# Kernel tuning notes

Hardware: AMD Instinct MI355X
Metric: run time of the kernel (lower is better)

## Reference

```python
import jax, jax.numpy as jnp
import numpy as np
from itertools import combinations, product

NQ = 10
DIM = 2 ** NQ
DEPTH = 1
ENC_PAIRS = [(q, q + 1) for q in range(0, NQ - 1, 2)] + [(q, q + 1) for q in range(1, NQ - 1, 2)]  # brick layer: even then odd
PYR = [(i, i + 1) for layer in range(NQ - 1) for i in range(NQ - layer - 1)]  # pyramid RBS wire pairs (45)
OBS_PAIRS = list(combinations(range(NQ), 2))  # 45 pairwise 2-local observables

_P = {'I': np.eye(2, dtype=np.complex128),
      'X': np.array([[0, 1], [1, 0]], dtype=np.complex128),
      'Y': np.array([[0, -1j], [1j, 0]], dtype=np.complex128),
      'Z': np.array([[1, 0], [0, -1]], dtype=np.complex128)}
_WORDS = [''.join(w) for w in product('IXYZ', repeat=2)][1:]  # PennyLane pauli_basis order, identity excluded
P15 = jnp.asarray(np.stack([np.kron(_P[w[0]], _P[w[1]]) for w in _WORDS]).astype(np.complex64))
XXm = jnp.asarray(np.kron(_P['X'], _P['X']).astype(np.complex64))
YYm = jnp.asarray(np.kron(_P['Y'], _P['Y']).astype(np.complex64))
ZZm = jnp.asarray(np.kron(_P['Z'], _P['Z']).astype(np.complex64))
I4 = jnp.eye(4, dtype=jnp.complex64)
_TRIL_I, _TRIL_J = np.tril_indices(4, -1)  # order matches create_Hermitian's count+j indexing


def _u3(t, p, l):
    c = jnp.cos(t / 2).astype(jnp.complex64)
    s = jnp.sin(t / 2).astype(jnp.complex64)
    return jnp.stack([jnp.stack([c, -jnp.exp(1j * l) * s]),
                      jnp.stack([jnp.exp(1j * p) * s, jnp.exp(1j * (p + l)) * c])])


def _ising(phi, P):
    # exp(-i*phi/2 * P) for P in {XX, YY, ZZ} (P^2 = I)
    return jnp.cos(phi / 2) * I4 - 1j * jnp.sin(phi / 2) * P


def _apply1(psi, U, w):
    # psi: (B, 2, ..., 2); single-qubit gate U (2,2) on wire w
    psi = jnp.moveaxis(psi, 1 + w, -1)
    sh = psi.shape
    out = jnp.einsum('ij,brj->bri', U, psi.reshape(sh[0], -1, 2)).reshape(sh)
    return jnp.moveaxis(out, -1, 1 + w)


def _apply2(psi, U, a, b):
    # two-qubit gate on wires (a,b), a is most-significant (PennyLane wire order). U: (4,4) or batched (B,4,4)
    psi = jnp.moveaxis(psi, (1 + a, 1 + b), (-2, -1))
    sh = psi.shape
    flat = psi.reshape(sh[0], -1, 4)
    eq = 'bij,brj->bri' if U.ndim == 3 else 'ij,brj->bri'
    out = jnp.einsum(eq, U, flat).reshape(sh)
    return jnp.moveaxis(out, (-2, -1), (1 + a, 1 + b))


def _build_H(A, B, D):
    # create_Hermitian: lower triangle A+iB, diag[0:3] = D[1:4], diag[3]=0, then h + h^dagger
    n = A.shape[0]
    h = jnp.zeros((n, 4, 4), jnp.complex64)
    h = h.at[:, _TRIL_I, _TRIL_J].set(A.astype(jnp.complex64) + 1j * B.astype(jnp.complex64))
    d = np.arange(3)
    h = h.at[:, d, d].set(D[:, 1:4].astype(jnp.complex64))
    return h + jnp.conj(jnp.swapaxes(h, -1, -2))


def setup_inputs() -> dict:
    key = jax.random.key(0)
    ks = jax.random.split(key, 9)
    f32 = jnp.float32
    return {
        'x': jax.random.normal(ks[0], (256, 512), f32),
        'W1': jax.random.normal(ks[1], (512, 256), f32) * (512 ** -0.5),
        'b1': jnp.zeros((256,), f32),
        'W2': jax.random.normal(ks[2], (256, 135), f32) * (256 ** -0.5),
        'b2': jnp.zeros((135,), f32),
        'qvit_params': 0.01 * jax.random.normal(ks[3], (DEPTH, len(PYR), 12), f32),
        'A': 2.0 * jax.random.normal(ks[4], (len(OBS_PAIRS), 6), f32),
        'B': 2.0 * jax.random.normal(ks[5], (len(OBS_PAIRS), 6), f32),
        'D': 2.0 * jax.random.normal(ks[6], (len(OBS_PAIRS), 4), f32),
    }


def reference(x, W1, b1, W2, b2, qvit_params, A, B, D):
    Bsz = x.shape[0]
    # enc_proj: Linear -> SiLU -> Linear
    enc = jax.nn.silu(x @ W1 + b1) @ W2 + b2  # (B, 135)
    # Brick-layer SpecialUnitary encoding: U = exp(i * sum theta_m P_m) via eigh
    theta = enc.reshape(Bsz, len(ENC_PAIRS), 15).astype(jnp.complex64)
    Hg = jnp.einsum('bgm,mij->bgij', theta, P15)  # Hermitian generators (B, 9, 4, 4)
    ew, V = jnp.linalg.eigh(Hg)
    Ue = jnp.einsum('bgik,bgk,bgjk->bgij', V, jnp.exp(1j * ew.astype(jnp.complex64)), jnp.conj(V))
    # |0...0>
    psi = jnp.zeros((Bsz, DIM), jnp.complex64).at[:, 0].set(1.0).reshape((Bsz,) + (2,) * NQ)
    for g, (a, b) in enumerate(ENC_PAIRS):
        psi = _apply2(psi, Ue[:, g], a, b)
    # QViT pyramid ansatz
    for ly in range(DEPTH):
        for g, (a, b) in enumerate(PYR):
            p = qvit_params[ly, g]
            psi = _apply1(psi, _u3(p[0], p[1], p[2]), a)
            psi = _apply2(psi, _ising(p[3], XXm), a, b)
            psi = _apply2(psi, _ising(p[4], YYm), a, b)
            psi = _apply2(psi, _ising(p[5], ZZm), a, b)
            psi = _apply1(psi, _u3(p[6], p[7], p[8]), a)
            psi = _apply2(psi, _ising(p[9], XXm), a, b)
            psi = _apply2(psi, _ising(p[10], YYm), a, b)
            psi = _apply2(psi, _ising(p[11], ZZm), a, b)
    # Pairwise ANO Hermitian expectations
    Hobs = _build_H(A, B, D)  # (45, 4, 4)
    outs = []
    for w, (a, b) in enumerate(OBS_PAIRS):
        pm = jnp.moveaxis(psi, (1 + a, 1 + b), (1, 2)).reshape(Bsz, 4, -1)
        outs.append(jnp.real(jnp.einsum('bir,ij,bjr->b', jnp.conj(pm), Hobs[w], pm)))
    return jnp.stack(outs, axis=1).astype(jnp.float32)
```

## Files before the change

### kernel.cpp

```cpp
#include <hip/hip_runtime.h>
#include <math.h>

#define NOBS 45
typedef float2 c32;

__device__ __constant__ int PA_s[NOBS] = {
    1,1,1,1,1,1,1,1,1, 0,0,0,0,0,0,0,0, 7,7,7,7,7,7,7, 6,6,6,6,6,6,
    5,5,5,5,5, 3,3,3,3, 2,2,2, 4,4, 9};
__device__ __constant__ int PB_s[NOBS] = {
    0,7,6,5,3,2,4,9,8, 7,6,5,3,2,4,9,8, 6,5,3,2,4,9,8, 5,3,2,4,9,8,
    3,2,4,9,8, 2,4,9,8, 4,9,8, 9,8, 8};
constexpr int TIc[6] = {1, 2, 2, 3, 3, 3};
constexpr int TJc[6] = {0, 0, 1, 0, 1, 2};

__device__ __forceinline__ c32 cfma(c32 a, c32 b, c32 c) {
    c.x = fmaf(a.x, b.x, fmaf(-a.y, b.y, c.x));
    c.y = fmaf(a.x, b.y, fmaf(a.y, b.x, c.y));
    return c;
}
__device__ __forceinline__ c32 cmul(c32 a, c32 b) {
    return make_float2(a.x * b.x - a.y * b.y, a.x * b.y + a.y * b.x);
}

template <int CTRL>
__device__ __forceinline__ float dppf(float x) {
    return __uint_as_float((unsigned)__builtin_amdgcn_update_dpp(
        0, (int)__float_as_uint(x), CTRL, 0xF, 0xF, true));
}
__device__ __forceinline__ float swap32f(float a) {
    auto r = __builtin_amdgcn_permlane32_swap(__float_as_uint(a), __float_as_uint(a), false, false);
    return (__uint_as_float(r[0]) + __uint_as_float(r[1])) - a;
}
#if __has_builtin(__builtin_amdgcn_permlane16_swap)
__device__ __forceinline__ float swap16f(float a) {
    auto r = __builtin_amdgcn_permlane16_swap(__float_as_uint(a), __float_as_uint(a), false, false);
    return (__uint_as_float(r[0]) + __uint_as_float(r[1])) - a;
}
#else
__device__ __forceinline__ float swap16f(float a) { return __shfl_xor(a, 16, 64); }
#endif
__device__ __forceinline__ float swz4f(float a) {
    return __uint_as_float(__builtin_amdgcn_ds_swizzle(__float_as_uint(a), 0x101F));
}
template <int M>
__device__ __forceinline__ float exf(float x) {
    float r = x;
    if constexpr ((M & 3) == 1) r = dppf<0xB1>(r);
    else if constexpr ((M & 3) == 2) r = dppf<0x4E>(r);
    else if constexpr ((M & 3) == 3) r = dppf<0x1B>(r);
    if constexpr (M & 4)  r = swz4f(r);
    if constexpr (M & 8)  r = dppf<0x128>(r);
    if constexpr (M & 16) r = swap16f(r);
    if constexpr (M & 32) r = swap32f(r);
    return r;
}
template <int M>
__device__ __forceinline__ c32 exch(c32 a) { return make_float2(exf<M>(a.x), exf<M>(a.y)); }
__device__ __forceinline__ c32 swap32c(c32 a) { return make_float2(swap32f(a.x), swap32f(a.y)); }

__device__ __forceinline__ float wave_reduce63(float x) {
    x += dppf<0x111>(x);
    x += dppf<0x112>(x);
    x += dppf<0x114>(x);
    x += dppf<0x118>(x);
    x += dppf<0x142>(x);
    x += dppf<0x143>(x);
    return x;
}

__device__ __forceinline__ int insert2(int t, int pl, int ph) {
    int low  = t & ((1 << pl) - 1);
    int rest = t >> pl;
    int nm   = ph - 1 - pl;
    int mid  = rest & ((1 << nm) - 1);
    int high = rest >> nm;
    return low | (mid << (pl + 1)) | (high << (ph + 1));
}

template <int W>
__device__ __forceinline__ c32 pE(int r, int c) {
    if constexpr (W == 0) return make_float2((r == c) ? 1.f : 0.f, 0.f);
    else if constexpr (W == 1) return make_float2((r != c) ? 1.f : 0.f, 0.f);
    else if constexpr (W == 2) return make_float2(0.f, (r == c) ? 0.f : ((r == 0) ? -1.f : 1.f));
    else return make_float2((r == c) ? ((r == 0) ? 1.f : -1.f) : 0.f, 0.f);
}
template <int W0, int W1>
__device__ __forceinline__ void paccum(c32& H, float th, int i1, int i2, int j1, int j2) {
    c32 a = pE<W0>(i1, j1), b = pE<W1>(i2, j2);
    c32 p = cmul(a, b);
    H.x = fmaf(th, p.x, H.x);
    H.y = fmaf(th, p.y, H.y);
}

struct F16 { c32 u[16]; };
struct FLoc { c32 a[4]; c32 b[4]; };
struct F4 { c32 uS, uB, uA, uC; };

__device__ __forceinline__ F16 loadF16(const c32* __restrict__ U) {
    F16 f;
#pragma unroll
    for (int i = 0; i < 16; i++) f.u[i] = U[i];
    return f;
}
__device__ __forceinline__ FLoc loadLoc(const c32* __restrict__ U, int ln) {
    int bb = (ln >> 5) & 1;
    const c32* U0 = U + bb * 4;
    const c32* U1 = U + (2 | bb) * 4;
    int c00 = bb, c01 = 2 | bb, c10 = bb ^ 1, c11 = 2 | (bb ^ 1);
    FLoc f;
    f.a[0] = U0[c00]; f.a[1] = U0[c01]; f.a[2] = U0[c10]; f.a[3] = U0[c11];
    f.b[0] = U1[c00]; f.b[1] = U1[c01]; f.b[2] = U1[c10]; f.b[3] = U1[c11];
    return f;
}
template <int QA, int QB>
__device__ __forceinline__ F4 loadL2(const c32* __restrict__ U, int ln) {
    int bA = (ln >> QA) & 1, bB = (ln >> QB) & 1;
    int r = (bA << 1) | bB;
    const c32* Ur = U + r * 4;
    F4 f;
    f.uS = Ur[r]; f.uB = Ur[r ^ 1]; f.uA = Ur[r ^ 2]; f.uC = Ur[r ^ 3];
    return f;
}

__device__ __forceinline__ void applyLL(c32 v[4], const F16& f) {
    c32 n0 = cfma(f.u[0],  v[0], cfma(f.u[1],  v[1], cfma(f.u[2],  v[2], cmul(f.u[3],  v[3]))));
    c32 n1 = cfma(f.u[4],  v[0], cfma(f.u[5],  v[1], cfma(f.u[6],  v[2], cmul(f.u[7],  v[3]))));
    c32 n2 = cfma(f.u[8],  v[0], cfma(f.u[9],  v[1], cfma(f.u[10], v[2], cmul(f.u[11], v[3]))));
    c32 n3 = cfma(f.u[12], v[0], cfma(f.u[13], v[1], cfma(f.u[14], v[2], cmul(f.u[15], v[3]))));
    v[0] = n0; v[1] = n1; v[2] = n2; v[3] = n3;
}
__device__ __forceinline__ void applyLoc(c32 v[4], const FLoc& f) {
    c32 p0 = swap32c(v[0]), p1 = swap32c(v[1]), p2 = swap32c(v[2]), p3 = swap32c(v[3]);
    c32 n0 = cfma(f.a[0], v[0], cfma(f.a[1], v[1], cfma(f.a[2], p0, cmul(f.a[3], p1))));
    c32 n1 = cfma(f.b[0], v[0], cfma(f.b[1], v[1], cfma(f.b[2], p0, cmul(f.b[3], p1))));
    c32 n2 = cfma(f.a[0], v[2], cfma(f.a[1], v[3], cfma(f.a[2], p2, cmul(f.a[3], p3))));
    c32 n3 = cfma(f.b[0], v[2], cfma(f.b[1], v[3], cfma(f.b[2], p2, cmul(f.b[3], p3))));
    v[0] = n0; v[1] = n1; v[2] = n2; v[3] = n3;
}
template <int QA, int QB>
__device__ __forceinline__ void applyL2(c32 v[4], const F4& f) {
#pragma unroll
    for (int lc = 0; lc < 4; lc++) {
        c32 pB = exch<(1 << QB)>(v[lc]);
        c32 pA = exch<(1 << QA)>(v[lc]);
        c32 pC = exch<(1 << QA)>(pB);
        v[lc] = cfma(f.uS, v[lc], cfma(f.uB, pB, cfma(f.uA, pA, cmul(f.uC, pC))));
    }
}

__device__ __forceinline__ void dumpV(const c32 v[4], c32* __restrict__ psi, int t) {
#pragma unroll
    for (int lc = 0; lc < 4; lc++) psi[(t << 2) | lc] = v[lc];
}
__device__ __forceinline__ void loadV(c32 v[4], const c32* __restrict__ psi, int t) {
#pragma unroll
    for (int lc = 0; lc < 4; lc++) v[lc] = psi[(t << 2) | lc];
}
template <int PA, int PB>
__device__ __forceinline__ void ldsApply(const F16& f, c32* __restrict__ psi, int t) {
    constexpr int PL = (PA < PB) ? PA : PB, PH = (PA < PB) ? PB : PA;
    int base = insert2(t, PL, PH);
    constexpr int oa = 1 << PA, ob = 1 << PB;
    c32 g0 = psi[base], g1 = psi[base + ob], g2 = psi[base + oa], g3 = psi[base + oa + ob];
    c32 n0 = cfma(f.u[0],  g0, cfma(f.u[1],  g1, cfma(f.u[2],  g2, cmul(f.u[3],  g3))));
    c32 n1 = cfma(f.u[4],  g0, cfma(f.u[5],  g1, cfma(f.u[6],  g2, cmul(f.u[7],  g3))));
    c32 n2 = cfma(f.u[8],  g0, cfma(f.u[9],  g1, cfma(f.u[10], g2, cmul(f.u[11], g3))));
    c32 n3 = cfma(f.u[12], g0, cfma(f.u[13], g1, cfma(f.u[14], g2, cmul(f.u[15], g3))));
    psi[base] = n0; psi[base + ob] = n1; psi[base + oa] = n2; psi[base + oa + ob] = n3;
}

__global__ __launch_bounds__(256, 1) void mega_kernel(
    const float* __restrict__ x,  const float* __restrict__ W1, const float* __restrict__ b1,
    const float* __restrict__ W2, const float* __restrict__ b2, const float* __restrict__ qp,
    const float* __restrict__ Am, const float* __restrict__ Bm, const float* __restrict__ Dm,
    float* __restrict__ out) {
    __shared__ __align__(16) c32 psiS[1024];
    __shared__ c32 UeS[144];
    __shared__ c32 GpS[720];
    __shared__ float HbS[720];
    __shared__ float encS[136];
    __shared__ float redS[180];

    const int b = blockIdx.x, t = threadIdx.x, ln = t & 63;
    float* F = (float*)psiS;

    if (t < 128) ((float4*)F)[t] = ((const float4*)(x + (size_t)b * 512))[t];
    __syncthreads();
    {
        int q = t & 63, sl = t >> 6;
        float4 a4 = make_float4(0.f, 0.f, 0.f, 0.f);
#pragma unroll 16
        for (int kk = 0; kk < 128; kk++) {
            int k = sl * 128 + kk;
            float xk = F[k];
            const float4 w = *(const float4*)(W1 + (size_t)k * 256 + q * 4);
            a4.x = fmaf(xk, w.x, a4.x); a4.y = fmaf(xk, w.y, a4.y);
            a4.z = fmaf(xk, w.z, a4.z); a4.w = fmaf(xk, w.w, a4.w);
        }
        *(float4*)(F + 512 + sl * 256 + q * 4) = a4;
    }
    __syncthreads();
    {
        float hv = b1[t] + F[512 + t] + F[768 + t] + F[1024 + t] + F[1280 + t];
        hv = hv / (1.f + __expf(-hv));
        F[1536 + t] = hv;
    }
    __syncthreads();
    if (t < 135) {
        float a2 = b2[t], a3 = 0.f;
#pragma unroll 16
        for (int k = 0; k < 128; k++) {
            a2 = fmaf(F[1536 + k],       W2[(size_t)k * 135 + t],         a2);
            a3 = fmaf(F[1536 + 128 + k], W2[(size_t)(128 + k) * 135 + t], a3);
        }
        encS[t] = a2 + a3;
    }
    __syncthreads();

    c32* Mm = psiS;
    c32* Rb = psiS + 144;
    c32* TA = psiS + 288;
    if (t < 144) {
        int m = t >> 4, e = t & 15, i = e >> 2, j = e & 3;
        int i1 = i >> 1, i2 = i & 1, j1 = j >> 1, j2 = j & 1;
        const float* th = encS + m * 15;
        c32 H = make_float2(0.f, 0.f);
        paccum<0,1>(H, th[0],  i1,i2,j1,j2); paccum<0,2>(H, th[1],  i1,i2,j1,j2);
        paccum<0,3>(H, th[2],  i1,i2,j1,j2); paccum<1,0>(H, th[3],  i1,i2,j1,j2);
        paccum<1,1>(H, th[4],  i1,i2,j1,j2); paccum<1,2>(H, th[5],  i1,i2,j1,j2);
        paccum<1,3>(H, th[6],  i1,i2,j1,j2); paccum<2,0>(H, th[7],  i1,i2,j1,j2);
        paccum<2,1>(H, th[8],  i1,i2,j1,j2); paccum<2,2>(H, th[9],  i1,i2,j1,j2);
        paccum<2,3>(H, th[10], i1,i2,j1,j2); paccum<3,0>(H, th[11], i1,i2,j1,j2);
        paccum<3,1>(H, th[12], i1,i2,j1,j2); paccum<3,2>(H, th[13], i1,i2,j1,j2);
        paccum<3,3>(H, th[14], i1,i2,j1,j2);
        const float sc = 1.f / 64.f;
        Mm[t] = make_float2(-H.y * sc, H.x * sc);
        Rb[t] = make_float2((i == j) ? 1.f : 0.f, 0.f);
    } else if (t >= 234) {
        for (int w = t - 234; w < NOBS; w += 22) {
            float* Hf = HbS + w * 16;
            Hf[0] = 2.f * Dm[w * 4 + 1];
            Hf[1] = 2.f * Dm[w * 4 + 2];
            Hf[2] = 2.f * Dm[w * 4 + 3];
            Hf[3] = 0.f;
#pragma unroll
            for (int k = 0; k < 6; k++) {
                Hf[4 + 2 * k] = 2.f * Am[w * 6 + k];
                Hf[5 + 2 * k] = 2.f * Bm[w * 6 + k];
            }
        }
    }
    __syncthreads();
    c32 Mrow[4];
    if (t < 144) {
        int m = t >> 4, i = (t & 15) >> 2;
#pragma unroll
        for (int k = 0; k < 4; k++) Mrow[k] = Mm[m * 16 + i * 4 + k];
    }
#pragma unroll 1
    for (int step = 0; step < 13; step++) {
        if (t < 144) {
            int m = t >> 4, e = t & 15, i = e >> 2, j = e & 3;
            const c32* cur = (step & 1) ? UeS : Rb;
            c32 acc = make_float2(0.f, 0.f);
            c32 outv;
            if (step < 7) {
#pragma unroll
                for (int k = 0; k < 4; k++) acc = cfma(Mrow[k], cur[m * 16 + k * 4 + j], acc);
                float inv = 1.f / (float)(7 - step);
                outv = make_float2(fmaf(acc.x, inv, (i == j) ? 1.f : 0.f), acc.y * inv);
            } else {
#pragma unroll
                for (int k = 0; k < 4; k++)
                    acc = cfma(cur[m * 16 + i * 4 + k], cur[m * 16 + k * 4 + j], acc);
                outv = acc;
            }
            ((step & 1) ? Rb : UeS)[t] = outv;
        } else if (t >= 144 && t < 234 && step < 8) {
            int pt = t - 144, g = pt >> 1, ih = (pt & 1) << 1;
            const float* p = qp + g * 12;
            const c32* src = ((step & 1) ? TA : GpS) + g * 16;
            c32* dst = ((step & 1) ? GpS : TA) + g * 16;
#pragma unroll
            for (int r2 = 0; r2 < 2; r2++) {
                int i = ih + r2, i1 = i >> 1, i2 = i & 1;
                c32 row[4];
                if (step == 0) {
                    float s, c; __sincosf(p[0] * 0.5f, &s, &c);
                    c32 u0, u1;
                    if (i1 == 0) { u0 = make_float2(c, 0.f);
                                   u1 = make_float2(-__cosf(p[2]) * s, -__sinf(p[2]) * s); }
                    else { u0 = make_float2(__cosf(p[1]) * s, __sinf(p[1]) * s);
                           u1 = make_float2(__cosf(p[1] + p[2]) * c, __sinf(p[1] + p[2]) * c); }
#pragma unroll
                    for (int jj = 0; jj < 4; jj++) row[jj] = make_float2(0.f, 0.f);
                    row[i2] = u0; row[2 | i2] = u1;
                } else {
                    c32 coef0, coef1; int c0, c1;
                    if (step == 1 || step == 5) {
                        float s, c; __sincosf(p[step == 1 ? 3 : 9] * 0.5f, &s, &c);
                        c0 = i; coef0 = make_float2(c, 0.f);
                        c1 = i ^ 3; coef1 = make_float2(0.f, -s);
                    } else if (step == 2 || step == 6) {
                        float s, c; __sincosf(p[step == 2 ? 4 : 10] * 0.5f, &s, &c);
                        float yy = (i == 0 || i == 3) ? 1.f : -1.f;
                        c0 = i; coef0 = make_float2(c, 0.f);
                        c1 = i ^ 3; coef1 = make_float2(0.f, s * yy);
                    } else if (step == 3 || step == 7) {
                        float s, c; __sincosf(p[step == 3 ? 5 : 11] * 0.5f, &s, &c);
                        float zz = (i == 0 || i == 3) ? 1.f : -1.f;
                        c0 = i; coef0 = make_float2(c, -s * zz);
                        c1 = i; coef1 = make_float2(0.f, 0.f);
                    } else {
                        float s, c; __sincosf(p[6] * 0.5f, &s, &c);
                        if (i1 == 0) { coef0 = make_float2(c, 0.f);
                                       coef1 = make_float2(-__cosf(p[8]) * s, -__sinf(p[8]) * s); }
                        else { coef0 = make_float2(__cosf(p[7]) * s, __sinf(p[7]) * s);
                               coef1 = make_float2(__cosf(p[7] + p[8]) * c, __sinf(p[7] + p[8]) * c); }
                        c0 = i2; c1 = 2 | i2;
                    }
#pragma unroll
                    for (int jj = 0; jj < 4; jj++)
                        row[jj] = cfma(coef0, src[c0 * 4 + jj], cmul(coef1, src[c1 * 4 + jj]));
                }
#pragma unroll
                for (int jj = 0; jj < 4; jj++) dst[i * 4 + jj] = row[jj];
            }
        }
        __syncthreads();
    }

    c32 v[4];
#pragma unroll
    for (int lc = 0; lc < 4; lc++) v[lc] = make_float2(0.f, 0.f);
    if (t == 0) v[0] = make_float2(1.f, 0.f);

    applyLL(v, loadF16(UeS + 0));
    applyL2<5, 4>(v, loadL2<5, 4>(UeS + 16, ln));
    applyL2<3, 1>(v, loadL2<3, 1>(UeS + 32, ln));
    applyL2<0, 2>(v, loadL2<0, 2>(UeS + 48, ln));
    dumpV(v, psiS, t); __syncthreads();
    ldsApply<9, 8>(loadF16(UeS + 64), psiS, t); __syncthreads();
    loadV(v, psiS, t);
    applyLoc(v, loadLoc(UeS + 80, ln));
    applyL2<4, 3>(v, loadL2<4, 3>(UeS + 96, ln));
    applyL2<1, 0>(v, loadL2<1, 0>(UeS + 112, ln));
    dumpV(v, psiS, t); __syncthreads();
    ldsApply<4, 9>(loadF16(UeS + 128), psiS, t); __syncthreads();
    loadV(v, psiS, t);

    {
        int g = 0;
#pragma unroll 1
        for (int layer = 0; layer < 9; layer++) {
            const int amax = 8 - layer;
            applyLL(v, loadF16(GpS + (g++) * 16));
            if (amax >= 1) applyLoc(v, loadLoc(GpS + (g++) * 16, ln));
            if (amax >= 2) applyL2<5, 4>(v, loadL2<5, 4>(GpS + (g++) * 16, ln));
            if (amax >= 3) applyL2<4, 3>(v, loadL2<4, 3>(GpS + (g++) * 16, ln));
            if (amax >= 4) applyL2<3, 1>(v, loadL2<3, 1>(GpS + (g++) * 16, ln));
            if (amax >= 5) applyL2<1, 0>(v, loadL2<1, 0>(GpS + (g++) * 16, ln));
            if (amax >= 6) applyL2<0, 2>(v, loadL2<0, 2>(GpS + (g++) * 16, ln));
            if (amax >= 7) {
                dumpV(v, psiS, t); __syncthreads();
                ldsApply<4, 9>(loadF16(GpS + (g++) * 16), psiS, t); __syncthreads();
                if (amax >= 8) {
                    ldsApply<9, 8>(loadF16(GpS + (g++) * 16), psiS, t); __syncthreads();
                }
                loadV(v, psiS, t);
            }
        }
    }

    dumpV(v, psiS, t);
    __syncthreads();
#pragma unroll 1
    for (int w0 = 0; w0 < NOBS; w0 += 5) {
        float pr[5];
#pragma unroll
        for (int u = 0; u < 5; u++) {
            const int w = w0 + u;
            const int pa = PA_s[w], pb = PB_s[w];
            const int pl = (pa < pb) ? pa : pb, phh = (pa < pb) ? pb : pa;
            const int oa = 1 << pa, ob = 1 << pb;
            int i0 = insert2(t, pl, phh);
            c32 vg[4];
            vg[0] = psiS[i0];      vg[1] = psiS[i0 + ob];
            vg[2] = psiS[i0 + oa]; vg[3] = psiS[i0 + oa + ob];
            const float* Hf = HbS + w * 16;
            float r = Hf[0] * fmaf(vg[0].x, vg[0].x, vg[0].y * vg[0].y)
                    + Hf[1] * fmaf(vg[1].x, vg[1].x, vg[1].y * vg[1].y)
                    + Hf[2] * fmaf(vg[2].x, vg[2].x, vg[2].y * vg[2].y);
#pragma unroll
            for (int k = 0; k < 6; k++) {
                c32 vi = vg[TIc[k]], vj = vg[TJc[k]];
                float cx = fmaf(vi.x, vj.x, vi.y * vj.y);
                float cy = fmaf(vi.x, vj.y, -vi.y * vj.x);
                r = fmaf(Hf[4 + 2 * k], cx, r);
                r = fmaf(-Hf[5 + 2 * k], cy, r);
            }
            pr[u] = wave_reduce63(r);
        }
        if (ln == 63) {
#pragma unroll
            for (int u = 0; u < 5; u++) redS[(w0 + u) * 4 + (t >> 6)] = pr[u];
        }
    }
    __syncthreads();
    if (t < NOBS)
        out[(size_t)b * NOBS + t] = redS[t * 4] + redS[t * 4 + 1] + redS[t * 4 + 2] + redS[t * 4 + 3];
}

extern "C" void kernel_launch(void* const* d_in, const int* in_sizes, int n_in,
                              void* d_out, int out_size, void* d_ws, size_t ws_size,
                              hipStream_t stream) {
    (void)in_sizes; (void)n_in; (void)out_size; (void)d_ws; (void)ws_size;
    const float* x  = (const float*)d_in[0];
    const float* W1 = (const float*)d_in[1];
    const float* b1 = (const float*)d_in[2];
    const float* W2 = (const float*)d_in[3];
    const float* b2 = (const float*)d_in[4];
    const float* qp = (const float*)d_in[5];
    const float* Am = (const float*)d_in[6];
    const float* Bm = (const float*)d_in[7];
    const float* Dm = (const float*)d_in[8];
    float* out = (float*)d_out;

    hipLaunchKernelGGL(mega_kernel, dim3(256), dim3(256), 0, stream,
                       x, W1, b1, W2, b2, qp, Am, Bm, Dm, out);
}
```

Before: 112.2 us.

## Process two batch rows per 512-thread block and fully unroll gate and observable loops

Each block now handles two batch elements, one per 256-thread half. The two halves keep separate state-vector, encoder-unitary and reduction buffers in LDS but share the pyramid gate matrices, which are built once per block. The grid drops from 256 blocks to 128, which spreads the gate setup over two rows and puts more waves on each CU, but leaves half the CUs idle on a 256-CU device. The pyramid layer loop and the observable loop are also fully unrolled, with the qubit-pair indices now compile-time constants instead of constant-memory lookups. That unrolling makes the code larger.

```diff
diff --git a/kernel.cpp b/kernel.cpp
--- a/kernel.cpp
+++ b/kernel.cpp
@@ -4,12 +4,13 @@
 #define NOBS 45
 typedef float2 c32;
 
-__device__ __constant__ int PA_s[NOBS] = {
-    1,1,1,1,1,1,1,1,1, 0,0,0,0,0,0,0,0, 7,7,7,7,7,7,7, 6,6,6,6,6,6,
-    5,5,5,5,5, 3,3,3,3, 2,2,2, 4,4, 9};
-__device__ __constant__ int PB_s[NOBS] = {
-    0,7,6,5,3,2,4,9,8, 7,6,5,3,2,4,9,8, 6,5,3,2,4,9,8, 5,3,2,4,9,8,
-    3,2,4,9,8, 2,4,9,8, 4,9,8, 9,8, 8};
+constexpr int W2Sc[10] = {1, 0, 7, 6, 5, 3, 2, 4, 9, 8};
+constexpr int OAc[NOBS] = {
+    0,0,0,0,0,0,0,0,0, 1,1,1,1,1,1,1,1, 2,2,2,2,2,2,2, 3,3,3,3,3,3,
+    4,4,4,4,4, 5,5,5,5, 6,6,6, 7,7, 8};
+constexpr int OBc[NOBS] = {
+    1,2,3,4,5,6,7,8,9, 2,3,4,5,6,7,8,9, 3,4,5,6,7,8,9, 4,5,6,7,8,9,
+    5,6,7,8,9, 6,7,8,9, 7,8,9, 8,9, 9};
 constexpr int TIc[6] = {1, 2, 2, 3, 3, 3};
 constexpr int TJc[6] = {0, 0, 1, 0, 1, 2};
 
@@ -148,18 +149,18 @@
     }
 }
 
-__device__ __forceinline__ void dumpV(const c32 v[4], c32* __restrict__ psi, int t) {
-#pragma unroll
-    for (int lc = 0; lc < 4; lc++) psi[(t << 2) | lc] = v[lc];
-}
-__device__ __forceinline__ void loadV(c32 v[4], const c32* __restrict__ psi, int t) {
-#pragma unroll
-    for (int lc = 0; lc < 4; lc++) v[lc] = psi[(t << 2) | lc];
+__device__ __forceinline__ void dumpV(const c32 v[4], c32* __restrict__ psi, int tt) {
+#pragma unroll
+    for (int lc = 0; lc < 4; lc++) psi[(tt << 2) | lc] = v[lc];
+}
+__device__ __forceinline__ void loadV(c32 v[4], const c32* __restrict__ psi, int tt) {
+#pragma unroll
+    for (int lc = 0; lc < 4; lc++) v[lc] = psi[(tt << 2) | lc];
 }
 template <int PA, int PB>
-__device__ __forceinline__ void ldsApply(const F16& f, c32* __restrict__ psi, int t) {
+__device__ __forceinline__ void ldsApply(const F16& f, c32* __restrict__ psi, int tt) {
     constexpr int PL = (PA < PB) ? PA : PB, PH = (PA < PB) ? PB : PA;
-    int base = insert2(t, PL, PH);
+    int base = insert2(tt, PL, PH);
     constexpr int oa = 1 << PA, ob = 1 << PB;
     c32 g0 = psi[base], g1 = psi[base + ob], g2 = psi[base + oa], g3 = psi[base + oa + ob];
     c32 n0 = cfma(f.u[0],  g0, cfma(f.u[1],  g1, cfma(f.u[2],  g2, cmul(f.u[3],  g3))));
@@ -169,25 +170,28 @@
     psi[base] = n0; psi[base + ob] = n1; psi[base + oa] = n2; psi[base + oa + ob] = n3;
 }
 
-__global__ __launch_bounds__(256, 1) void mega_kernel(
+__global__ __launch_bounds__(512, 2) void mega_kernel(
     const float* __restrict__ x,  const float* __restrict__ W1, const float* __restrict__ b1,
     const float* __restrict__ W2, const float* __restrict__ b2, const float* __restrict__ qp,
     const float* __restrict__ Am, const float* __restrict__ Bm, const float* __restrict__ Dm,
     float* __restrict__ out) {
-    __shared__ __align__(16) c32 psiS[1024];
-    __shared__ c32 UeS[144];
+    __shared__ __align__(16) c32 psiS[2048];
+    __shared__ c32 UeS[288];
     __shared__ c32 GpS[720];
     __shared__ float HbS[720];
-    __shared__ float encS[136];
-    __shared__ float redS[180];
-
-    const int b = blockIdx.x, t = threadIdx.x, ln = t & 63;
-    float* F = (float*)psiS;
-
-    if (t < 128) ((float4*)F)[t] = ((const float4*)(x + (size_t)b * 512))[t];
+    __shared__ float encS[2][136];
+    __shared__ float redS[2][180];
+
+    const int t = threadIdx.x, elem = t >> 8, tt = t & 255, ln = t & 63;
+    const int row = blockIdx.x * 2 + elem;
+    c32* psiE = psiS + (elem << 10);
+    c32* UeE  = UeS + elem * 144;
+    float* F = (float*)psiE;
+
+    if (tt < 128) ((float4*)F)[tt] = ((const float4*)(x + (size_t)row * 512))[tt];
     __syncthreads();
     {
-        int q = t & 63, sl = t >> 6;
+        int q = tt & 63, sl = tt >> 6;
         float4 a4 = make_float4(0.f, 0.f, 0.f, 0.f);
 #pragma unroll 16
         for (int kk = 0; kk < 128; kk++) {
@@ -201,29 +205,29 @@
     }
     __syncthreads();
     {
-        float hv = b1[t] + F[512 + t] + F[768 + t] + F[1024 + t] + F[1280 + t];
+        float hv = b1[tt] + F[512 + tt] + F[768 + tt] + F[1024 + tt] + F[1280 + tt];
         hv = hv / (1.f + __expf(-hv));
-        F[1536 + t] = hv;
-    }
-    __syncthreads();
-    if (t < 135) {
-        float a2 = b2[t], a3 = 0.f;
+        F[1536 + tt] = hv;
+    }
+    __syncthreads();
+    if (tt < 135) {
+        float a2 = b2[tt], a3 = 0.f;
 #pragma unroll 16
         for (int k = 0; k < 128; k++) {
-            a2 = fmaf(F[1536 + k],       W2[(size_t)k * 135 + t],         a2);
-            a3 = fmaf(F[1536 + 128 + k], W2[(size_t)(128 + k) * 135 + t], a3);
-        }
-        encS[t] = a2 + a3;
-    }
-    __syncthreads();
-
-    c32* Mm = psiS;
-    c32* Rb = psiS + 144;
+            a2 = fmaf(F[1536 + k],       W2[(size_t)k * 135 + tt],         a2);
+            a3 = fmaf(F[1536 + 128 + k], W2[(size_t)(128 + k) * 135 + tt], a3);
+        }
+        encS[elem][tt] = a2 + a3;
+    }
+    __syncthreads();
+
+    c32* Mm = psiE;
+    c32* Rb = psiE + 144;
     c32* TA = psiS + 288;
-    if (t < 144) {
-        int m = t >> 4, e = t & 15, i = e >> 2, j = e & 3;
+    if (tt < 144) {
+        int m = tt >> 4, e = tt & 15, i = e >> 2, j = e & 3;
         int i1 = i >> 1, i2 = i & 1, j1 = j >> 1, j2 = j & 1;
-        const float* th = encS + m * 15;
+        const float* th = encS[elem] + m * 15;
         c32 H = make_float2(0.f, 0.f);
         paccum<0,1>(H, th[0],  i1,i2,j1,j2); paccum<0,2>(H, th[1],  i1,i2,j1,j2);
         paccum<0,3>(H, th[2],  i1,i2,j1,j2); paccum<1,0>(H, th[3],  i1,i2,j1,j2);
@@ -234,10 +238,10 @@
         paccum<3,1>(H, th[12], i1,i2,j1,j2); paccum<3,2>(H, th[13], i1,i2,j1,j2);
         paccum<3,3>(H, th[14], i1,i2,j1,j2);
         const float sc = 1.f / 64.f;
-        Mm[t] = make_float2(-H.y * sc, H.x * sc);
-        Rb[t] = make_float2((i == j) ? 1.f : 0.f, 0.f);
-    } else if (t >= 234) {
-        for (int w = t - 234; w < NOBS; w += 22) {
+        Mm[tt] = make_float2(-H.y * sc, H.x * sc);
+        Rb[tt] = make_float2((i == j) ? 1.f : 0.f, 0.f);
+    } else if (elem == 0 && tt >= 234) {
+        for (int w = tt - 234; w < NOBS; w += 22) {
             float* Hf = HbS + w * 16;
             Hf[0] = 2.f * Dm[w * 4 + 1];
             Hf[1] = 2.f * Dm[w * 4 + 2];
@@ -252,16 +256,16 @@
     }
     __syncthreads();
     c32 Mrow[4];
-    if (t < 144) {
-        int m = t >> 4, i = (t & 15) >> 2;
+    if (tt < 144) {
+        int m = tt >> 4, i = (tt & 15) >> 2;
 #pragma unroll
         for (int k = 0; k < 4; k++) Mrow[k] = Mm[m * 16 + i * 4 + k];
     }
 #pragma unroll 1
     for (int step = 0; step < 13; step++) {
-        if (t < 144) {
-            int m = t >> 4, e = t & 15, i = e >> 2, j = e & 3;
-            const c32* cur = (step & 1) ? UeS : Rb;
+        if (tt < 144) {
+            int m = tt >> 4, e = tt & 15, i = e >> 2, j = e & 3;
+            const c32* cur = (step & 1) ? UeE : Rb;
             c32 acc = make_float2(0.f, 0.f);
             c32 outv;
             if (step < 7) {
@@ -275,16 +279,16 @@
                     acc = cfma(cur[m * 16 + i * 4 + k], cur[m * 16 + k * 4 + j], acc);
                 outv = acc;
             }
-            ((step & 1) ? Rb : UeS)[t] = outv;
-        } else if (t >= 144 && t < 234 && step < 8) {
-            int pt = t - 144, g = pt >> 1, ih = (pt & 1) << 1;
+            ((step & 1) ? Rb : UeE)[tt] = outv;
+        } else if (elem == 0 && tt >= 144 && tt < 234 && step < 8) {
+            int pt = tt - 144, g = pt >> 1, ih = (pt & 1) << 1;
             const float* p = qp + g * 12;
             const c32* src = ((step & 1) ? TA : GpS) + g * 16;
             c32* dst = ((step & 1) ? GpS : TA) + g * 16;
 #pragma unroll
             for (int r2 = 0; r2 < 2; r2++) {
                 int i = ih + r2, i1 = i >> 1, i2 = i & 1;
-                c32 row[4];
+                c32 rowv[4];
                 if (step == 0) {
                     float s, c; __sincosf(p[0] * 0.5f, &s, &c);
                     c32 u0, u1;
@@ -293,8 +297,8 @@
                     else { u0 = make_float2(__cosf(p[1]) * s, __sinf(p[1]) * s);
                            u1 = make_float2(__cosf(p[1] + p[2]) * c, __sinf(p[1] + p[2]) * c); }
 #pragma unroll
-                    for (int jj = 0; jj < 4; jj++) row[jj] = make_float2(0.f, 0.f);
-                    row[i2] = u0; row[2 | i2] = u1;
+                    for (int jj = 0; jj < 4; jj++) rowv[jj] = make_float2(0.f, 0.f);
+                    rowv[i2] = u0; rowv[2 | i2] = u1;
                 } else {
                     c32 coef0, coef1; int c0, c1;
                     if (step == 1 || step == 5) {
@@ -321,10 +325,10 @@
                     }
 #pragma unroll
                     for (int jj = 0; jj < 4; jj++)
-                        row[jj] = cfma(coef0, src[c0 * 4 + jj], cmul(coef1, src[c1 * 4 + jj]));
+                        rowv[jj] = cfma(coef0, src[c0 * 4 + jj], cmul(coef1, src[c1 * 4 + jj]));
                 }
 #pragma unroll
-                for (int jj = 0; jj < 4; jj++) dst[i * 4 + jj] = row[jj];
+                for (int jj = 0; jj < 4; jj++) dst[i * 4 + jj] = rowv[jj];
             }
         }
         __syncthreads();
@@ -333,25 +337,25 @@
     c32 v[4];
 #pragma unroll
     for (int lc = 0; lc < 4; lc++) v[lc] = make_float2(0.f, 0.f);
-    if (t == 0) v[0] = make_float2(1.f, 0.f);
-
-    applyLL(v, loadF16(UeS + 0));
-    applyL2<5, 4>(v, loadL2<5, 4>(UeS + 16, ln));
-    applyL2<3, 1>(v, loadL2<3, 1>(UeS + 32, ln));
-    applyL2<0, 2>(v, loadL2<0, 2>(UeS + 48, ln));
-    dumpV(v, psiS, t); __syncthreads();
-    ldsApply<9, 8>(loadF16(UeS + 64), psiS, t); __syncthreads();
-    loadV(v, psiS, t);
-    applyLoc(v, loadLoc(UeS + 80, ln));
-    applyL2<4, 3>(v, loadL2<4, 3>(UeS + 96, ln));
-    applyL2<1, 0>(v, loadL2<1, 0>(UeS + 112, ln));
-    dumpV(v, psiS, t); __syncthreads();
-    ldsApply<4, 9>(loadF16(UeS + 128), psiS, t); __syncthreads();
-    loadV(v, psiS, t);
+    if (tt == 0) v[0] = make_float2(1.f, 0.f);
+
+    applyLL(v, loadF16(UeE + 0));
+    applyL2<5, 4>(v, loadL2<5, 4>(UeE + 16, ln));
+    applyL2<3, 1>(v, loadL2<3, 1>(UeE + 32, ln));
+    applyL2<0, 2>(v, loadL2<0, 2>(UeE + 48, ln));
+    dumpV(v, psiE, tt); __syncthreads();
+    ldsApply<9, 8>(loadF16(UeE + 64), psiE, tt); __syncthreads();
+    loadV(v, psiE, tt);
+    applyLoc(v, loadLoc(UeE + 80, ln));
+    applyL2<4, 3>(v, loadL2<4, 3>(UeE + 96, ln));
+    applyL2<1, 0>(v, loadL2<1, 0>(UeE + 112, ln));
+    dumpV(v, psiE, tt); __syncthreads();
+    ldsApply<4, 9>(loadF16(UeE + 128), psiE, tt); __syncthreads();
+    loadV(v, psiE, tt);
 
     {
         int g = 0;
-#pragma unroll 1
+#pragma unroll
         for (int layer = 0; layer < 9; layer++) {
             const int amax = 8 - layer;
             applyLL(v, loadF16(GpS + (g++) * 16));
@@ -362,31 +366,31 @@
             if (amax >= 5) applyL2<1, 0>(v, loadL2<1, 0>(GpS + (g++) * 16, ln));
             if (amax >= 6) applyL2<0, 2>(v, loadL2<0, 2>(GpS + (g++) * 16, ln));
             if (amax >= 7) {
-                dumpV(v, psiS, t); __syncthreads();
-                ldsApply<4, 9>(loadF16(GpS + (g++) * 16), psiS, t); __syncthreads();
+                dumpV(v, psiE, tt); __syncthreads();
+                ldsApply<4, 9>(loadF16(GpS + (g++) * 16), psiE, tt); __syncthreads();
                 if (amax >= 8) {
-                    ldsApply<9, 8>(loadF16(GpS + (g++) * 16), psiS, t); __syncthreads();
+                    ldsApply<9, 8>(loadF16(GpS + (g++) * 16), psiE, tt); __syncthreads();
                 }
-                loadV(v, psiS, t);
+                loadV(v, psiE, tt);
             }
         }
     }
 
-    dumpV(v, psiS, t);
-    __syncthreads();
-#pragma unroll 1
+    dumpV(v, psiE, tt);
+    __syncthreads();
+#pragma unroll
     for (int w0 = 0; w0 < NOBS; w0 += 5) {
         float pr[5];
 #pragma unroll
         for (int u = 0; u < 5; u++) {
             const int w = w0 + u;
-            const int pa = PA_s[w], pb = PB_s[w];
+            const int pa = W2Sc[OAc[w]], pb = W2Sc[OBc[w]];
             const int pl = (pa < pb) ? pa : pb, phh = (pa < pb) ? pb : pa;
             const int oa = 1 << pa, ob = 1 << pb;
-            int i0 = insert2(t, pl, phh);
+            int i0 = insert2(tt, pl, phh);
             c32 vg[4];
-            vg[0] = psiS[i0];      vg[1] = psiS[i0 + ob];
-            vg[2] = psiS[i0 + oa]; vg[3] = psiS[i0 + oa + ob];
+            vg[0] = psiE[i0];      vg[1] = psiE[i0 + ob];
+            vg[2] = psiE[i0 + oa]; vg[3] = psiE[i0 + oa + ob];
             const float* Hf = HbS + w * 16;
             float r = Hf[0] * fmaf(vg[0].x, vg[0].x, vg[0].y * vg[0].y)
                     + Hf[1] * fmaf(vg[1].x, vg[1].x, vg[1].y * vg[1].y)
@@ -403,12 +407,13 @@
         }
         if (ln == 63) {
 #pragma unroll
-            for (int u = 0; u < 5; u++) redS[(w0 + u) * 4 + (t >> 6)] = pr[u];
-        }
-    }
-    __syncthreads();
-    if (t < NOBS)
-        out[(size_t)b * NOBS + t] = redS[t * 4] + redS[t * 4 + 1] + redS[t * 4 + 2] + redS[t * 4 + 3];
+            for (int u = 0; u < 5; u++) redS[elem][(w0 + u) * 4 + (tt >> 6)] = pr[u];
+        }
+    }
+    __syncthreads();
+    if (tt < NOBS)
+        out[(size_t)row * NOBS + tt] = redS[elem][tt * 4] + redS[elem][tt * 4 + 1]
+                                     + redS[elem][tt * 4 + 2] + redS[elem][tt * 4 + 3];
 }
 
 extern "C" void kernel_launch(void* const* d_in, const int* in_sizes, int n_in,
@@ -426,6 +431,6 @@
     const float* Dm = (const float*)d_in[8];
     float* out = (float*)d_out;
 
-    hipLaunchKernelGGL(mega_kernel, dim3(256), dim3(256), 0, stream,
+    hipLaunchKernelGGL(mega_kernel, dim3(128), dim3(512), 0, stream,
                        x, W1, b1, W2, b2, qp, Am, Bm, Dm, out);
 }
```

Measured after the change: 121.3 us. 8.0% more time.
